# Kernel optimization log

Hardware: AMD Instinct MI355X
Metric: run time of the kernel (lower is better)

## Reference

```python
import jax, jax.numpy as jnp
import numpy as np

B, S, D, H, KH, DH, L, V, MULT = 1, 2048, 2048, 16, 2, 128, 4, 10000, 4
INNER = D * MULT
EPS = 1e-5


def layernorm(x, g, b):
    m = jnp.mean(x, axis=-1, keepdims=True)
    v = jnp.var(x, axis=-1, keepdims=True)
    return (x - m) * jax.lax.rsqrt(v + EPS) * g + b


def setup_inputs() -> dict:
    key = jax.random.key(0)
    ks = jax.random.split(key, 24)
    s = lambda *shape: 0.02
    inp = {
        'text': jax.random.randint(ks[0], (B, S), 0, V),
        'embed_w': jax.random.normal(ks[1], (V, D), jnp.float32) * 0.02,
        # model-level LayerNorm (applied after embed and after every block)
        'model_norm_g': jnp.ones((D,), jnp.float32),
        'model_norm_b': jnp.zeros((D,), jnp.float32),
        # per-block params, stacked on leading L axis
        'blk_norm_g': jnp.ones((L, D), jnp.float32),
        'blk_norm_b': jnp.zeros((L, D), jnp.float32),
        'attn_norm_g': jnp.ones((L, D), jnp.float32),  # RingAttention prenorm
        'attn_norm_b': jnp.zeros((L, D), jnp.float32),
        'wq': jax.random.normal(ks[2], (L, D, H * DH), jnp.float32) * 0.02,
        'wk': jax.random.normal(ks[3], (L, D, KH * DH), jnp.float32) * 0.02,
        'wv': jax.random.normal(ks[4], (L, D, KH * DH), jnp.float32) * 0.02,
        'wo': jax.random.normal(ks[5], (L, H * DH, D), jnp.float32) * 0.02,
        'qn_g': jnp.ones((L, DH), jnp.float32),  # qk_norm LayerNorm scales
        'kn_g': jnp.ones((L, DH), jnp.float32),
        'w1': jax.random.normal(ks[6], (L, D, INNER), jnp.float32) * 0.02,
        'b1': jnp.zeros((L, INNER), jnp.float32),
        'w2': jax.random.normal(ks[7], (L, INNER, D), jnp.float32) * 0.02,
        'b2': jnp.zeros((L, D), jnp.float32),
        # output head: LayerNorm + Linear(D, V)
        'head_norm_g': jnp.ones((D,), jnp.float32),
        'head_norm_b': jnp.zeros((D,), jnp.float32),
        'head_w': jax.random.normal(ks[8], (D, V), jnp.float32) * 0.02,
        'head_b': jnp.zeros((V,), jnp.float32),
    }
    return inp


def _attention(xn, wq, wk, wv, wo, qn_g, kn_g):
    # xn: [B,S,D] (already prenormed)
    q = (xn @ wq).reshape(B, S, H, DH)
    k = (xn @ wk).reshape(B, S, KH, DH)
    v = (xn @ wv).reshape(B, S, KH, DH)
    # qk-norm: LayerNorm over head dim with learnable scale
    q = layernorm(q, qn_g, 0.0)
    k = layernorm(k, kn_g, 0.0)
    # GQA: expand kv heads to query heads
    rep = H // KH
    k = jnp.repeat(k, rep, axis=2)  # [B,S,H,DH]
    v = jnp.repeat(v, rep, axis=2)
    scale = DH ** -0.5
    scores = jnp.einsum('bqhd,bkhd->bhqk', q, k) * scale  # [B,H,S,S]
    causal = jnp.tril(jnp.ones((S, S), bool))
    scores = jnp.where(causal, scores, jnp.finfo(scores.dtype).min)
    p = jax.nn.softmax(scores, axis=-1)
    out = jnp.einsum('bhqk,bkhd->bqhd', p, v).reshape(B, S, H * DH)
    return out @ wo


def reference(text, embed_w, model_norm_g, model_norm_b, blk_norm_g, blk_norm_b,
              attn_norm_g, attn_norm_b, wq, wk, wv, wo, qn_g, kn_g,
              w1, b1, w2, b2, head_norm_g, head_norm_b, head_w, head_b):
    x = embed_w[text]                                # [B,S,D]
    x = layernorm(x, model_norm_g, model_norm_b)
    for i in range(L):
        h = layernorm(x, blk_norm_g[i], blk_norm_b[i])       # block norm
        hn = layernorm(h, attn_norm_g[i], attn_norm_b[i])    # attn prenorm
        h = _attention(hn, wq[i], wk[i], wv[i], wo[i], qn_g[i], kn_g[i]) + h
        ff = jax.nn.gelu(h @ w1[i] + b1[i]) @ w2[i] + b2[i]
        x = ff + h
        x = layernorm(x, model_norm_g, model_norm_b)
    x = layernorm(x, head_norm_g, head_norm_b)
    return x @ head_w + head_b                       # [B,S,V] logits
```

## Files before the change

kernel.cpp:

```cpp
#include <hip/hip_runtime.h>
#include <math.h>

#define S_LEN 2048
#define DMODEL 2048
#define NHEAD 16
#define KVHEAD 2
#define DHEAD 128
#define NLAYER 4
#define VOCAB 10000
#define INNER_DIM 8192
#define LN_EPS 1e-5f
#define VOCAB_PAD 10240
#define QKVN 2560

typedef __attribute__((ext_vector_type(4))) float f32x4;
typedef __attribute__((ext_vector_type(2))) float f32x2;
typedef __attribute__((ext_vector_type(8))) short s16x8;
typedef __attribute__((ext_vector_type(4))) short s16x4;

__device__ __forceinline__ short f2bf(float f) {
  union { float f; unsigned u; } v; v.f = f;
  unsigned r = v.u + 0x7FFFu + ((v.u >> 16) & 1u);
  return (short)(r >> 16);
}
__device__ __forceinline__ float bf2f(short s) {
  union { unsigned u; float f; } v; v.u = ((unsigned)(unsigned short)s) << 16;
  return v.f;
}

__device__ __forceinline__ float gelu_tanh(float x) {
  float z = 0.7978845608028654f * (x + 0.044715f * x * x * x);
  float t = __expf(-2.0f * fabsf(z));
  float th = (1.0f - t) / (1.0f + t);
  th = copysignf(th, z);
  return 0.5f * x * (1.0f + th);
}

__device__ __forceinline__ void glds16(const void* g, void* l) {
  __builtin_amdgcn_global_load_lds(
      (const __attribute__((address_space(1))) unsigned int*)g,
      (__attribute__((address_space(3))) unsigned int*)l, 16, 0, 0);
}

__global__ __launch_bounds__(256)
void wtrans_all(const float* __restrict__ wq, const float* __restrict__ wk,
                const float* __restrict__ wv, const float* __restrict__ wo,
                const float* __restrict__ w1, const float* __restrict__ w2,
                short* __restrict__ wqkvT, short* __restrict__ woT,
                short* __restrict__ w1T, short* __restrict__ w2T) {
  __shared__ float ld[64][65];
  int b = blockIdx.x;
  const float* W; short* WT; int gx, K;
  if (b < 1024)      { W = wq; WT = wqkvT; gx = 32; K = 2048; }
  else if (b < 1152) { b -= 1024; W = wk; WT = wqkvT + (size_t)2048 * 2048; gx = 4; K = 2048; }
  else if (b < 1280) { b -= 1152; W = wv; WT = wqkvT + (size_t)2304 * 2048; gx = 4; K = 2048; }
  else if (b < 2304) { b -= 1280; W = wo; WT = woT; gx = 32; K = 2048; }
  else if (b < 6400) { b -= 2304; W = w1; WT = w1T; gx = 128; K = 2048; }
  else               { b -= 6400; W = w2; WT = w2T; gx = 32; K = 8192; }
  const int N = gx * 64;
  const int n0 = (b % gx) * 64, k0 = (b / gx) * 64;
  const int tid = threadIdx.x;
  const int rbase = tid >> 4;
  const int c4 = (tid & 15) * 4;
#pragma unroll
  for (int q = 0; q < 4; ++q) {
    int kk = rbase + q * 16;
    f32x4 v = *(const f32x4*)(W + (size_t)(k0 + kk) * N + n0 + c4);
    ld[kk][c4 + 0] = v[0]; ld[kk][c4 + 1] = v[1];
    ld[kk][c4 + 2] = v[2]; ld[kk][c4 + 3] = v[3];
  }
  __syncthreads();
#pragma unroll
  for (int s = 0; s < 2; ++s) {
    int lin = tid + s * 256;
    int nn = lin >> 3;
    int ks = lin & 7;
    s16x8 o;
#pragma unroll
    for (int j = 0; j < 8; ++j) o[j] = f2bf(ld[ks * 8 + j][nn]);
    *(s16x8*)&WT[(size_t)(n0 + nn) * K + k0 + ks * 8] = o;
  }
}

__global__ __launch_bounds__(256)
void wtrans64(const float* __restrict__ W, short* __restrict__ WT,
              int K, int N, int NP) {
  __shared__ float ld[64][65];
  const int n0 = blockIdx.x * 64, k0 = blockIdx.y * 64;
  const int tid = threadIdx.x;
  const int rbase = tid >> 4;
  const int c4 = (tid & 15) * 4;
#pragma unroll
  for (int q = 0; q < 4; ++q) {
    int kk = rbase + q * 16;
    const float* wp = W + (size_t)(k0 + kk) * N + n0 + c4;
    float v0, v1, v2, v3;
    if (n0 + c4 + 3 < N) {
      f32x4 v = *(const f32x4*)wp;
      v0 = v[0]; v1 = v[1]; v2 = v[2]; v3 = v[3];
    } else {
      v0 = (n0 + c4 + 0 < N) ? wp[0] : 0.f;
      v1 = (n0 + c4 + 1 < N) ? wp[1] : 0.f;
      v2 = (n0 + c4 + 2 < N) ? wp[2] : 0.f;
      v3 = (n0 + c4 + 3 < N) ? wp[3] : 0.f;
    }
    ld[kk][c4 + 0] = v0; ld[kk][c4 + 1] = v1;
    ld[kk][c4 + 2] = v2; ld[kk][c4 + 3] = v3;
  }
  __syncthreads();
#pragma unroll
  for (int s = 0; s < 2; ++s) {
    int lin = tid + s * 256;
    int nn = lin >> 3;
    int ks = lin & 7;
    int n = n0 + nn;
    if (n < NP) {
      s16x8 o;
#pragma unroll
      for (int j = 0; j < 8; ++j)
        o[j] = (n < N) ? f2bf(ld[ks * 8 + j][nn]) : (short)0;
      *(s16x8*)&WT[(size_t)n * K + k0 + ks * 8] = o;
    }
  }
}

__device__ __forceinline__ void ln3_core(
    float (&v)[8], int tid, int wave,
    const float* __restrict__ mg, const float* __restrict__ mb,
    const float* __restrict__ bg, const float* __restrict__ bb,
    const float* __restrict__ ag, const float* __restrict__ ab,
    short* __restrict__ hbrow, short* __restrict__ hnrow,
    float rs[3][4], float rs2[3][4]) {
#pragma unroll
  for (int rnd = 0; rnd < 3; ++rnd) {
    float s = 0.f, s2 = 0.f;
#pragma unroll
    for (int i = 0; i < 8; ++i) { s += v[i]; s2 += v[i] * v[i]; }
#pragma unroll
    for (int off = 1; off < 64; off <<= 1) {
      s += __shfl_xor(s, off); s2 += __shfl_xor(s2, off);
    }
    if ((tid & 63) == 0) { rs[rnd][wave] = s; rs2[rnd][wave] = s2; }
    __syncthreads();
    s = rs[rnd][0] + rs[rnd][1] + rs[rnd][2] + rs[rnd][3];
    s2 = rs2[rnd][0] + rs2[rnd][1] + rs2[rnd][2] + rs2[rnd][3];
    const float mean = s * (1.f / DMODEL);
    const float var = s2 * (1.f / DMODEL) - mean * mean;
    const float rstd = rsqrtf(var + LN_EPS);
    const float* gg = (rnd == 0) ? mg : (rnd == 1) ? bg : ag;
    const float* bbv = (rnd == 0) ? mb : (rnd == 1) ? bb : ab;
#pragma unroll
    for (int i = 0; i < 8; ++i) {
      int idx = tid + i * 256;
      v[i] = (v[i] - mean) * rstd * gg[idx] + bbv[idx];
    }
    if (rnd == 1) {
#pragma unroll
      for (int i = 0; i < 8; ++i) hbrow[tid + i * 256] = f2bf(v[i]);
    }
  }
#pragma unroll
  for (int i = 0; i < 8; ++i) hnrow[tid + i * 256] = f2bf(v[i]);
}

__global__ __launch_bounds__(256)
void embed_ln3(const int* __restrict__ text, const float* __restrict__ ew,
               const float* __restrict__ mg, const float* __restrict__ mb,
               const float* __restrict__ bg, const float* __restrict__ bb,
               const float* __restrict__ ag, const float* __restrict__ ab,
               short* __restrict__ hb16, short* __restrict__ hn16) {
  const int row = blockIdx.x;
  const int tid = threadIdx.x;
  const int wave = tid >> 6;
  __shared__ float rs[3][4], rs2[3][4];
  float v[8];
  const float* x = ew + (size_t)text[row] * DMODEL;
#pragma unroll
  for (int i = 0; i < 8; ++i) v[i] = x[tid + i * 256];
  ln3_core(v, tid, wave, mg, mb, bg, bb, ag, ab,
           hb16 + (size_t)row * DMODEL, hn16 + (size_t)row * DMODEL, rs, rs2);
}

__global__ __launch_bounds__(256)
void ln_triple_sum(const float* __restrict__ p0, const float* __restrict__ p1,
                   const short* __restrict__ h216, const float* __restrict__ b2,
                   const float* __restrict__ mg, const float* __restrict__ mb,
                   const float* __restrict__ bg, const float* __restrict__ bb,
                   const float* __restrict__ ag, const float* __restrict__ ab,
                   short* __restrict__ hb16, short* __restrict__ hn16) {
  const int row = blockIdx.x;
  const int tid = threadIdx.x;
  const int wave = tid >> 6;
  __shared__ float rs[3][4], rs2[3][4];
  float v[8];
  const size_t base = (size_t)row * DMODEL;
#pragma unroll
  for (int i = 0; i < 8; ++i) {
    int idx = tid + i * 256;
    v[i] = p0[base + idx] + p1[base + idx] + b2[idx] + bf2f(h216[base + idx]);
  }
  ln3_core(v, tid, wave, mg, mb, bg, bb, ag, ab,
           hb16 + base, hn16 + base, rs, rs2);
}

__global__ __launch_bounds__(256)
void ln_dual_sum(const float* __restrict__ p0, const float* __restrict__ p1,
                 const short* __restrict__ h216, const float* __restrict__ b2,
                 const float* __restrict__ mg, const float* __restrict__ mb,
                 const float* __restrict__ hg, const float* __restrict__ hbv,
                 short* __restrict__ out16) {
  const int row = blockIdx.x;
  const int tid = threadIdx.x;
  const int wave = tid >> 6;
  __shared__ float rs[2][4], rs2[2][4];
  float v[8];
  const size_t base = (size_t)row * DMODEL;
#pragma unroll
  for (int i = 0; i < 8; ++i) {
    int idx = tid + i * 256;
    v[i] = p0[base + idx] + p1[base + idx] + b2[idx] + bf2f(h216[base + idx]);
  }
#pragma unroll
  for (int rnd = 0; rnd < 2; ++rnd) {
    float s = 0.f, s2 = 0.f;
#pragma unroll
    for (int i = 0; i < 8; ++i) { s += v[i]; s2 += v[i] * v[i]; }
#pragma unroll
    for (int off = 1; off < 64; off <<= 1) {
      s += __shfl_xor(s, off); s2 += __shfl_xor(s2, off);
    }
    if ((tid & 63) == 0) { rs[rnd][wave] = s; rs2[rnd][wave] = s2; }
    __syncthreads();
    s = rs[rnd][0] + rs[rnd][1] + rs[rnd][2] + rs[rnd][3];
    s2 = rs2[rnd][0] + rs2[rnd][1] + rs2[rnd][2] + rs2[rnd][3];
    const float mean = s * (1.f / DMODEL);
    const float var = s2 * (1.f / DMODEL) - mean * mean;
    const float rstd = rsqrtf(var + LN_EPS);
    const float* gg = (rnd == 0) ? mg : hg;
    const float* bbv = (rnd == 0) ? mb : hbv;
#pragma unroll
    for (int i = 0; i < 8; ++i) {
      int idx = tid + i * 256;
      v[i] = (v[i] - mean) * rstd * gg[idx] + bbv[idx];
    }
  }
  short* o = out16 + base;
#pragma unroll
  for (int i = 0; i < 8; ++i) o[tid + i * 256] = f2bf(v[i]);
}

template<int BM, int BN, int BK, int WM, int WN, int ACT, bool BIAS, bool RESB,
         bool WF, bool WB, bool SPLITK>
__global__ __launch_bounds__(WM * WN * 64)
void gemm_db(const short* __restrict__ A, const short* __restrict__ BT,
             const float* __restrict__ bias, const short* __restrict__ res16,
             float* __restrict__ Cf, short* __restrict__ Cb,
             int M, int N, int K, int LDA, int LDB) {
  constexpr int THREADS = WM * WN * 64;
  constexpr int MR = BM / WM / 16;
  constexpr int NR = BN / WN / 16;
  constexpr int KH = BK / 32;
  constexpr int SLOTS = BK / 8;
  constexpr int SMASK = SLOTS - 1;
  constexpr int RSH = (SLOTS == 8) ? 0 : 1;
  constexpr int CSH = (SLOTS == 8) ? 3 : 2;
  constexpr int NIA = (BM * BK) / (THREADS * 8);
  constexpr int NIB = (BN * BK) / (THREADS * 8);
  __shared__ short As[2][BM * BK];
  __shared__ short Bs[2][BN * BK];
  const int tid = threadIdx.x;
  const int wave = tid >> 6, lane = tid & 63;
  const int g = lane >> 4, r = lane & 15;
  const int wm = wave / WN, wn = wave % WN;
  const int zoff = SPLITK ? blockIdx.z * K : 0;
  if (SPLITK && WF) Cf += (size_t)blockIdx.z * M * N;

  const int GY = gridDim.y;
  int lin = blockIdx.x + blockIdx.y * gridDim.x;
  int nwg = gridDim.x * GY;
  int sw = ((nwg & 7) == 0) ? ((lin & 7) * (nwg >> 3) + (lin >> 3)) : lin;
  const int bm = (sw % GY) * BM;
  const int bn = (sw / GY) * BN;

  const short* gsrc[NIA + NIB];
  short* ldst[2][NIA + NIB];
#pragma unroll
  for (int i = 0; i < NIA; ++i) {
    int c = i * THREADS + tid;
    int row = c >> CSH;
    int slot = c & SMASK;
    int col = ((slot ^ ((row >> RSH) & SMASK)) << 3);
    gsrc[i] = A + (size_t)(bm + row) * LDA + zoff + col;
    int base = (i * THREADS + (wave << 6)) << 3;
    ldst[0][i] = &As[0][base];
    ldst[1][i] = &As[1][base];
  }
#pragma unroll
  for (int i = 0; i < NIB; ++i) {
    int c = i * THREADS + tid;
    int row = c >> CSH;
    int slot = c & SMASK;
    int col = ((slot ^ ((row >> RSH) & SMASK)) << 3);
    gsrc[NIA + i] = BT + (size_t)(bn + row) * LDB + zoff + col;
    int base = (i * THREADS + (wave << 6)) << 3;
    ldst[0][NIA + i] = &Bs[0][base];
    ldst[1][NIA + i] = &Bs[1][base];
  }

  f32x4 acc[MR][NR] = {};
  const int NT = K / BK;

#pragma unroll
  for (int i = 0; i < NIA + NIB; ++i) glds16(gsrc[i], ldst[0][i]);
  asm volatile("s_waitcnt vmcnt(0)" ::: "memory");
  __syncthreads();

  for (int t = 0; t < NT; ++t) {
    const int cur = t & 1;
    const short* as = As[cur];
    const short* bs = Bs[cur];
    s16x8 bfr[NR][KH], af[(MR > 1) ? MR / 2 : 1][KH];
#pragma unroll
    for (int n = 0; n < NR; ++n) {
      int rr = wn * (NR * 16) + n * 16 + r;
#pragma unroll
      for (int kk = 0; kk < KH; ++kk) {
        int lg = kk * 4 + g;
        bfr[n][kk] = *(const s16x8*)&bs[rr * BK + ((lg ^ ((rr >> RSH) & SMASK)) << 3)];
      }
    }
#pragma unroll
    for (int mm = 0; mm < MR / 2; ++mm) {
      int rr = wm * (MR * 16) + mm * 16 + r;
#pragma unroll
      for (int kk = 0; kk < KH; ++kk) {
        int lg = kk * 4 + g;
        af[mm][kk] = *(const s16x8*)&as[rr * BK + ((lg ^ ((rr >> RSH) & SMASK)) << 3)];
      }
    }
    if (t + 1 < NT) {
#pragma unroll
      for (int i = 0; i < NIA + NIB; ++i) glds16(gsrc[i] + (t + 1) * BK, ldst[cur ^ 1][i]);
    }
    asm volatile("s_waitcnt lgkmcnt(0)" ::: "memory");
    __builtin_amdgcn_sched_barrier(0);
    __builtin_amdgcn_s_setprio(1);
#pragma unroll
    for (int mm = 0; mm < MR / 2; ++mm)
#pragma unroll
      for (int n = 0; n < NR; ++n)
#pragma unroll
        for (int kk = 0; kk < KH; ++kk)
          acc[mm][n] = __builtin_amdgcn_mfma_f32_16x16x32_bf16(af[mm][kk], bfr[n][kk], acc[mm][n], 0, 0, 0);
    __builtin_amdgcn_s_setprio(0);
    __builtin_amdgcn_s_barrier();
#pragma unroll
    for (int mm = 0; mm < MR / 2; ++mm) {
      int rr = wm * (MR * 16) + (MR / 2 + mm) * 16 + r;
#pragma unroll
      for (int kk = 0; kk < KH; ++kk) {
        int lg = kk * 4 + g;
        af[mm][kk] = *(const s16x8*)&as[rr * BK + ((lg ^ ((rr >> RSH) & SMASK)) << 3)];
      }
    }
    asm volatile("s_waitcnt lgkmcnt(0)" ::: "memory");
    __builtin_amdgcn_sched_barrier(0);
    __builtin_amdgcn_s_setprio(1);
#pragma unroll
    for (int mm = 0; mm < MR / 2; ++mm)
#pragma unroll
      for (int n = 0; n < NR; ++n)
#pragma unroll
        for (int kk = 0; kk < KH; ++kk)
          acc[MR / 2 + mm][n] = __builtin_amdgcn_mfma_f32_16x16x32_bf16(af[mm][kk], bfr[n][kk], acc[MR / 2 + mm][n], 0, 0, 0);
    __builtin_amdgcn_s_setprio(0);
    __syncthreads();
  }

#pragma unroll
  for (int m = 0; m < MR; ++m) {
    int row = bm + wm * (MR * 16) + m * 16 + g * 4;
#pragma unroll
    for (int n = 0; n < NR; ++n) {
      int col = bn + wn * (NR * 16) + n * 16 + r;
      if (col < N) {
#pragma unroll
        for (int j = 0; j < 4; ++j) {
          float v = acc[m][n][j];
          if (BIAS) v += bias[col];
          if (ACT) v = gelu_tanh(v);
          if (RESB) v += bf2f(res16[(size_t)(row + j) * N + col]);
          if (WF) Cf[(size_t)(row + j) * N + col] = v;
          if (WB) Cb[(size_t)(row + j) * N + col] = f2bf(v);
        }
      }
    }
  }
}

__global__ __launch_bounds__(256)
void gemm_qkv(const short* __restrict__ A, const short* __restrict__ BT,
              const float* __restrict__ qg, const float* __restrict__ kg,
              short* __restrict__ qb, short* __restrict__ kb,
              short* __restrict__ vt, int M, int K) {
  __shared__ short As[2][64 * 64];
  __shared__ short Bs[2][128 * 64];
  __shared__ float rsm[2][64], rs2m[2][64];
  const int tid = threadIdx.x;
  const int wave = tid >> 6, lane = tid & 63;
  const int g = lane >> 4, r = lane & 15;
  const int wm = wave >> 1, wn = wave & 1;

  const int GY = gridDim.y;
  int lin = blockIdx.x + blockIdx.y * gridDim.x;
  int nwg = gridDim.x * GY;
  int sw = (lin & 7) * (nwg >> 3) + (lin >> 3);
  const int bm = (sw % GY) * 64;
  const int bn = (sw / GY) * 128;

  const short* gsrc[6];
  short* ldst[2][6];
#pragma unroll
  for (int i = 0; i < 2; ++i) {
    int c = i * 256 + tid;
    int row = c >> 3, slot = c & 7;
    int col = ((slot ^ (row & 7)) << 3);
    gsrc[i] = A + (size_t)(bm + row) * K + col;
    int base = (i * 256 + (wave << 6)) << 3;
    ldst[0][i] = &As[0][base];
    ldst[1][i] = &As[1][base];
  }
#pragma unroll
  for (int i = 0; i < 4; ++i) {
    int c = i * 256 + tid;
    int row = c >> 3, slot = c & 7;
    int col = ((slot ^ (row & 7)) << 3);
    gsrc[2 + i] = BT + (size_t)(bn + row) * K + col;
    int base = (i * 256 + (wave << 6)) << 3;
    ldst[0][2 + i] = &Bs[0][base];
    ldst[1][2 + i] = &Bs[1][base];
  }

  f32x4 acc[2][4] = {};
  const int NT = K >> 6;

#pragma unroll
  for (int i = 0; i < 6; ++i) glds16(gsrc[i], ldst[0][i]);
  asm volatile("s_waitcnt vmcnt(0)" ::: "memory");
  __syncthreads();

  for (int t = 0; t < NT; ++t) {
    const int cur = t & 1;
    const short* as = As[cur];
    const short* bs = Bs[cur];
    s16x8 bfr[4][2], af[1][2];
#pragma unroll
    for (int n = 0; n < 4; ++n) {
      int rr = wn * 64 + n * 16 + r;
#pragma unroll
      for (int kk = 0; kk < 2; ++kk) {
        int lg = kk * 4 + g;
        bfr[n][kk] = *(const s16x8*)&bs[rr * 64 + ((lg ^ (rr & 7)) << 3)];
      }
    }
    {
      int rr = wm * 32 + r;
#pragma unroll
      for (int kk = 0; kk < 2; ++kk) {
        int lg = kk * 4 + g;
        af[0][kk] = *(const s16x8*)&as[rr * 64 + ((lg ^ (rr & 7)) << 3)];
      }
    }
    if (t + 1 < NT) {
#pragma unroll
      for (int i = 0; i < 6; ++i) glds16(gsrc[i] + (t + 1) * 64, ldst[cur ^ 1][i]);
    }
    asm volatile("s_waitcnt lgkmcnt(0)" ::: "memory");
    __builtin_amdgcn_sched_barrier(0);
    __builtin_amdgcn_s_setprio(1);
#pragma unroll
    for (int n = 0; n < 4; ++n)
#pragma unroll
      for (int kk = 0; kk < 2; ++kk)
        acc[0][n] = __builtin_amdgcn_mfma_f32_16x16x32_bf16(af[0][kk], bfr[n][kk], acc[0][n], 0, 0, 0);
    __builtin_amdgcn_s_setprio(0);
    __builtin_amdgcn_s_barrier();
    {
      int rr = wm * 32 + 16 + r;
#pragma unroll
      for (int kk = 0; kk < 2; ++kk) {
        int lg = kk * 4 + g;
        af[0][kk] = *(const s16x8*)&as[rr * 64 + ((lg ^ (rr & 7)) << 3)];
      }
    }
    asm volatile("s_waitcnt lgkmcnt(0)" ::: "memory");
    __builtin_amdgcn_sched_barrier(0);
    __builtin_amdgcn_s_setprio(1);
#pragma unroll
    for (int n = 0; n < 4; ++n)
#pragma unroll
      for (int kk = 0; kk < 2; ++kk)
        acc[1][n] = __builtin_amdgcn_mfma_f32_16x16x32_bf16(af[0][kk], bfr[n][kk], acc[1][n], 0, 0, 0);
    __builtin_amdgcn_s_setprio(0);
    __syncthreads();
  }

  if (bn >= 2304) {
    short* ld = &As[0][0];
#pragma unroll
    for (int m = 0; m < 2; ++m) {
      int sl = wm * 32 + m * 16 + g * 4;
#pragma unroll
      for (int n = 0; n < 4; ++n) {
        int dl = wn * 64 + n * 16 + r;
#pragma unroll
        for (int j = 0; j < 4; ++j)
          ld[(sl + j) * 128 + dl] = f2bf(acc[m][n][j]);
      }
    }
    __syncthreads();
    const int dl = tid & 127;
    const int sh = (tid >> 7) * 32;
    short* dst = vt + (size_t)(bn - 2304 + dl) * S_LEN + bm + sh;
#pragma unroll
    for (int v = 0; v < 4; ++v) {
      s16x8 o;
#pragma unroll
      for (int i = 0; i < 8; ++i) o[i] = ld[(sh + v * 8 + i) * 128 + dl];
      *(s16x8*)(dst + v * 8) = o;
    }
  } else {
    float ms[2][4], m2[2][4];
#pragma unroll
    for (int m = 0; m < 2; ++m)
#pragma unroll
      for (int j = 0; j < 4; ++j) {
        float s = 0.f, s2 = 0.f;
#pragma unroll
        for (int n = 0; n < 4; ++n) { float v = acc[m][n][j]; s += v; s2 += v * v; }
#pragma unroll
        for (int off = 1; off < 16; off <<= 1) {
          s += __shfl_xor(s, off); s2 += __shfl_xor(s2, off);
        }
        ms[m][j] = s; m2[m][j] = s2;
      }
    if (r == 0) {
#pragma unroll
      for (int m = 0; m < 2; ++m)
#pragma unroll
        for (int j = 0; j < 4; ++j) {
          int rl = wm * 32 + m * 16 + g * 4 + j;
          rsm[wn][rl] = ms[m][j]; rs2m[wn][rl] = m2[m][j];
        }
    }
    __syncthreads();
    const float* gv = (bn < 2048) ? qg : kg;
#pragma unroll
    for (int m = 0; m < 2; ++m)
#pragma unroll
      for (int j = 0; j < 4; ++j) {
        int rl = wm * 32 + m * 16 + g * 4 + j;
        float s = rsm[0][rl] + rsm[1][rl];
        float s2 = rs2m[0][rl] + rs2m[1][rl];
        float mean = s * (1.f / 128.f);
        float var = s2 * (1.f / 128.f) - mean * mean;
        float rstd = rsqrtf(var + LN_EPS);
        int srow = bm + rl;
#pragma unroll
        for (int n = 0; n < 4; ++n) {
          int cl = wn * 64 + n * 16 + r;
          float v = (acc[m][n][j] - mean) * rstd * gv[cl];
          if (bn < 2048) qb[(size_t)srow * 2048 + bn + cl] = f2bf(v);
          else kb[(size_t)srow * 256 + (bn - 2048) + cl] = f2bf(v);
        }
      }
  }
}

__global__ __launch_bounds__(256)
void attn_fwd3(const short* __restrict__ qbuf, const short* __restrict__ kbuf,
               const short* __restrict__ vtb, short* __restrict__ obuf) {
  __shared__ short Qs[64 * 128];
  __shared__ short Ks[64 * 128];
  __shared__ short Vt[128 * 64];
  __shared__ short Ps[4][16][88];
  const int tid = threadIdx.x;
  int lin = blockIdx.x + blockIdx.y * gridDim.x;
  int sw = (lin & 7) * 32 + (lin >> 3);
  const int pair = sw & 15;
  const int h = sw >> 4;
  const int kh = h >> 3;
  const int wave = tid >> 6, lane = tid & 63;
  const int g = lane >> 4, r = lane & 15;
  const float scale = 0.08838834764831845f;

#pragma unroll
  for (int half = 0; half < 2; ++half) {
    const int qt = half ? (31 - pair) : pair;
    const int qbase = qt * 64;
    __builtin_amdgcn_s_barrier();
#pragma unroll
    for (int i = 0; i < 4; ++i) {
      int c = i * 256 + tid;
      int row = c >> 4;
      int scol = (((c & 15) ^ (row & 7)) << 3);
      glds16(qbuf + (size_t)(qbase + row) * DMODEL + h * DHEAD + scol,
             &Qs[(i * 256 + (wave << 6)) << 3]);
    }
    f32x4 O[8] = {};
    float mst[4], lst[4];
#pragma unroll
    for (int j = 0; j < 4; ++j) { mst[j] = -1e30f; lst[j] = 0.f; }
    s16x8 aq[4];

    for (int jt = 0; jt <= qt; ++jt) {
      const int jb = jt * 64;
      if (jt) __builtin_amdgcn_s_barrier();
#pragma unroll
      for (int i = 0; i < 4; ++i) {
        int c = i * 256 + tid;
        int row = c >> 4;
        int scol = (((c & 15) ^ (row & 7)) << 3);
        glds16(kbuf + (size_t)(jb + row) * 256 + kh * DHEAD + scol,
               &Ks[(i * 256 + (wave << 6)) << 3]);
      }
#pragma unroll
      for (int i = 0; i < 4; ++i) {
        int c = i * 256 + tid;
        int row = c >> 3;
        int scol = (((c & 7) ^ (row & 7)) << 3);
        glds16(vtb + (size_t)(kh * 128 + row) * S_LEN + jb + scol,
               &Vt[(i * 256 + (wave << 6)) << 3]);
      }
      asm volatile("s_waitcnt vmcnt(4)" ::: "memory");
      __builtin_amdgcn_s_barrier();
      if (jt == 0) {
#pragma unroll
        for (int kc = 0; kc < 4; ++kc) {
          int rr = wave * 16 + r;
          aq[kc] = *(const s16x8*)&Qs[rr * 128 + ((((kc << 2) | g) ^ (rr & 7)) << 3)];
        }
      }
      f32x4 sc[4] = {};
      __builtin_amdgcn_s_setprio(1);
#pragma unroll
      for (int n = 0; n < 4; ++n) {
        int rr = n * 16 + r;
#pragma unroll
        for (int kc = 0; kc < 4; ++kc) {
          s16x8 bk = *(const s16x8*)&Ks[rr * 128 + ((((kc << 2) | g) ^ (rr & 7)) << 3)];
          sc[n] = __builtin_amdgcn_mfma_f32_16x16x32_bf16(aq[kc], bk, sc[n], 0, 0, 0);
        }
      }
      __builtin_amdgcn_s_setprio(0);
      if (jt == qt) {
#pragma unroll
        for (int j = 0; j < 4; ++j) {
          int irow = qbase + wave * 16 + g * 4 + j;
#pragma unroll
          for (int n = 0; n < 4; ++n) {
            int jcol = jb + n * 16 + r;
            sc[n][j] = (jcol <= irow) ? sc[n][j] * scale : -1e30f;
          }
        }
      } else {
#pragma unroll
        for (int j = 0; j < 4; ++j)
#pragma unroll
          for (int n = 0; n < 4; ++n) sc[n][j] *= scale;
      }
      float pmax[4], alpha[4], rsum[4];
#pragma unroll
      for (int j = 0; j < 4; ++j)
        pmax[j] = fmaxf(fmaxf(sc[0][j], sc[1][j]), fmaxf(sc[2][j], sc[3][j]));
#pragma unroll
      for (int off = 1; off < 16; off <<= 1)
#pragma unroll
        for (int j = 0; j < 4; ++j) pmax[j] = fmaxf(pmax[j], __shfl_xor(pmax[j], off));
#pragma unroll
      for (int j = 0; j < 4; ++j) {
        float mnew = fmaxf(mst[j], pmax[j]);
        alpha[j] = __expf(mst[j] - mnew);
        mst[j] = mnew;
#pragma unroll
        for (int n = 0; n < 4; ++n) sc[n][j] = __expf(sc[n][j] - mnew);
        rsum[j] = (sc[0][j] + sc[1][j]) + (sc[2][j] + sc[3][j]);
      }
#pragma unroll
      for (int off = 1; off < 16; off <<= 1)
#pragma unroll
        for (int j = 0; j < 4; ++j) rsum[j] += __shfl_xor(rsum[j], off);
#pragma unroll
      for (int j = 0; j < 4; ++j) lst[j] = lst[j] * alpha[j] + rsum[j];
#pragma unroll
      for (int d = 0; d < 8; ++d)
#pragma unroll
        for (int j = 0; j < 4; ++j) O[d][j] *= alpha[j];
      asm volatile("s_waitcnt vmcnt(0)" ::: "memory");
      __builtin_amdgcn_s_barrier();
#pragma unroll
      for (int j = 0; j < 4; ++j)
#pragma unroll
        for (int n = 0; n < 4; ++n)
          Ps[wave][g * 4 + j][n * 16 + r] = f2bf(sc[n][j]);
      s16x8 pa0 = *(const s16x8*)&Ps[wave][r][g * 8];
      s16x8 pa1 = *(const s16x8*)&Ps[wave][r][32 + g * 8];
      __builtin_amdgcn_s_setprio(1);
#pragma unroll
      for (int d = 0; d < 8; ++d) {
        int dd = d * 16 + r;
        s16x8 b0 = *(const s16x8*)&Vt[dd * 64 + ((g ^ (dd & 7)) << 3)];
        s16x8 b1 = *(const s16x8*)&Vt[dd * 64 + (((4 + g) ^ (dd & 7)) << 3)];
        O[d] = __builtin_amdgcn_mfma_f32_16x16x32_bf16(pa0, b0, O[d], 0, 0, 0);
        O[d] = __builtin_amdgcn_mfma_f32_16x16x32_bf16(pa1, b1, O[d], 0, 0, 0);
      }
      __builtin_amdgcn_s_setprio(0);
    }
    float linv[4];
#pragma unroll
    for (int j = 0; j < 4; ++j) linv[j] = 1.f / lst[j];
#pragma unroll
    for (int d = 0; d < 8; ++d)
#pragma unroll
      for (int j = 0; j < 4; ++j)
        obuf[(size_t)(qbase + wave * 16 + g * 4 + j) * DMODEL + h * DHEAD + d * 16 + r] =
            f2bf(O[d][j] * linv[j]);
  }
}

extern "C" void kernel_launch(void* const* d_in, const int* in_sizes, int n_in,
                              void* d_out, int out_size, void* d_ws, size_t ws_size,
                              hipStream_t stream) {
  const int* text = (const int*)d_in[0];
  const float* embed_w = (const float*)d_in[1];
  const float* model_g = (const float*)d_in[2];
  const float* model_b = (const float*)d_in[3];
  const float* blk_g = (const float*)d_in[4];
  const float* blk_b = (const float*)d_in[5];
  const float* attn_g = (const float*)d_in[6];
  const float* attn_b = (const float*)d_in[7];
  const float* wq = (const float*)d_in[8];
  const float* wk = (const float*)d_in[9];
  const float* wv = (const float*)d_in[10];
  const float* wo = (const float*)d_in[11];
  const float* qn_g = (const float*)d_in[12];
  const float* kn_g = (const float*)d_in[13];
  const float* w1 = (const float*)d_in[14];
  const float* b1 = (const float*)d_in[15];
  const float* w2 = (const float*)d_in[16];
  const float* b2 = (const float*)d_in[17];
  const float* head_g = (const float*)d_in[18];
  const float* head_b = (const float*)d_in[19];
  const float* head_w = (const float*)d_in[20];
  const float* head_bias = (const float*)d_in[21];
  float* out = (float*)d_out;

  const size_t SD = (size_t)S_LEN * DMODEL;
  const size_t SKV = (size_t)S_LEN * KVHEAD * DHEAD;
  const size_t SI = (size_t)S_LEN * INNER_DIM;
  const size_t WD = (size_t)DMODEL * DMODEL;
  const size_t WKV = (size_t)DMODEL * KVHEAD * DHEAD;
  const size_t WI = (size_t)DMODEL * INNER_DIM;

  char* p = (char*)d_ws;
  float* wpart = (float*)p; p += SD * 4 * 2;
  short* hb16  = (short*)p; p += SD * 2;
  short* hn16  = (short*)p; p += SD * 2;
  short* h216  = (short*)p; p += SD * 2;
  short* ao16  = (short*)p; p += SD * 2;
  short* ffi16 = (short*)p; p += SI * 2;
  short* qb16  = (short*)p; p += SD * 2;
  short* kb16  = (short*)p; p += SKV * 2;
  short* vt16  = (short*)p; p += SKV * 2;
  short* wqkvT = (short*)p; p += (size_t)QKVN * DMODEL * 2;
  short* woT   = (short*)p; p += WD * 2;
  short* w1T   = (short*)p; p += WI * 2;
  short* w2T   = (short*)p; p += WI * 2;
  short* headT = w1T;

  dim3 blk(256);
  embed_ln3<<<S_LEN, blk, 0, stream>>>(text, embed_w, model_g, model_b,
                                       blk_g, blk_b, attn_g, attn_b, hb16, hn16);

  for (int i = 0; i < NLAYER; ++i) {
    wtrans_all<<<10496, blk, 0, stream>>>(
        wq + (size_t)i * WD, wk + (size_t)i * WKV, wv + (size_t)i * WKV,
        wo + (size_t)i * WD, w1 + (size_t)i * WI, w2 + (size_t)i * WI,
        wqkvT, woT, w1T, w2T);

    gemm_qkv<<<dim3(QKVN / 128, S_LEN / 64), blk, 0, stream>>>(
        hn16, wqkvT, qn_g + i * DHEAD, kn_g + i * DHEAD,
        qb16, kb16, vt16, S_LEN, DMODEL);

    attn_fwd3<<<dim3(16, 16), blk, 0, stream>>>(qb16, kb16, vt16, ao16);

    gemm_db<64, 128, 64, 2, 2, 0, false, true, false, true, false>
        <<<dim3(DMODEL / 128, S_LEN / 64), blk, 0, stream>>>(
        ao16, woT, nullptr, hb16, nullptr, h216,
        S_LEN, DMODEL, DMODEL, DMODEL, DMODEL);
    gemm_db<128, 128, 64, 2, 2, 1, true, false, false, true, false>
        <<<dim3(INNER_DIM / 128, S_LEN / 128), blk, 0, stream>>>(
        h216, w1T, b1 + (size_t)i * INNER_DIM, nullptr, nullptr, ffi16,
        S_LEN, INNER_DIM, DMODEL, DMODEL, DMODEL);
    gemm_db<128, 128, 64, 2, 2, 0, false, false, true, false, true>
        <<<dim3(DMODEL / 128, S_LEN / 128, 2), blk, 0, stream>>>(
        ffi16, w2T, nullptr, nullptr, wpart, nullptr,
        S_LEN, DMODEL, INNER_DIM / 2, INNER_DIM, INNER_DIM);

    if (i + 1 < NLAYER) {
      ln_triple_sum<<<S_LEN, blk, 0, stream>>>(
          wpart, wpart + SD, h216, b2 + (size_t)i * DMODEL,
          model_g, model_b,
          blk_g + (i + 1) * DMODEL, blk_b + (i + 1) * DMODEL,
          attn_g + (i + 1) * DMODEL, attn_b + (i + 1) * DMODEL, hb16, hn16);
    } else {
      ln_dual_sum<<<S_LEN, blk, 0, stream>>>(
          wpart, wpart + SD, h216, b2 + (size_t)i * DMODEL,
          model_g, model_b, head_g, head_b, hn16);
    }
  }

  wtrans64<<<dim3(VOCAB_PAD / 64, 32), blk, 0, stream>>>(head_w, headT, DMODEL, VOCAB, VOCAB_PAD);
  gemm_db<128, 128, 64, 2, 2, 0, true, false, true, false, false>
      <<<dim3(VOCAB_PAD / 128, S_LEN / 128), blk, 0, stream>>>(
      hn16, headT, head_bias, nullptr, out, nullptr,
      S_LEN, VOCAB, DMODEL, DMODEL, DMODEL);
}
```

Measured before the change: 1.476 ms.

## Replace double-buffered GEMM LDS pipeline with single-buffer synchronous loads

Converts the GEMM kernels (generic and QKV) from double-buffered shared memory with prefetch of the next K tile overlapped with MFMA into a single buffer that loads, waits, syncs, then computes. It also drops the split A-fragment scheduling, setprio hints and sched barriers. The change halves LDS use, which could allow more resident workgroups per CU, but it removes overlap of global loads with compute and adds an extra barrier per iteration.

```diff
diff --git a/kernel.cpp b/kernel.cpp
--- a/kernel.cpp
+++ b/kernel.cpp
@@ -252,7 +252,7 @@
 template<int BM, int BN, int BK, int WM, int WN, int ACT, bool BIAS, bool RESB,
          bool WF, bool WB, bool SPLITK>
 __global__ __launch_bounds__(WM * WN * 64)
-void gemm_db(const short* __restrict__ A, const short* __restrict__ BT,
+void gemm_sb(const short* __restrict__ A, const short* __restrict__ BT,
              const float* __restrict__ bias, const short* __restrict__ res16,
              float* __restrict__ Cf, short* __restrict__ Cb,
              int M, int N, int K, int LDA, int LDB) {
@@ -266,8 +266,8 @@
   constexpr int CSH = (SLOTS == 8) ? 3 : 2;
   constexpr int NIA = (BM * BK) / (THREADS * 8);
   constexpr int NIB = (BN * BK) / (THREADS * 8);
-  __shared__ short As[2][BM * BK];
-  __shared__ short Bs[2][BN * BK];
+  __shared__ short As[BM * BK];
+  __shared__ short Bs[BN * BK];
   const int tid = threadIdx.x;
   const int wave = tid >> 6, lane = tid & 63;
   const int g = lane >> 4, r = lane & 15;
@@ -283,7 +283,7 @@
   const int bn = (sw / GY) * BN;
 
   const short* gsrc[NIA + NIB];
-  short* ldst[2][NIA + NIB];
+  short* ldst[NIA + NIB];
 #pragma unroll
   for (int i = 0; i < NIA; ++i) {
     int c = i * THREADS + tid;
@@ -291,9 +291,7 @@
     int slot = c & SMASK;
     int col = ((slot ^ ((row >> RSH) & SMASK)) << 3);
     gsrc[i] = A + (size_t)(bm + row) * LDA + zoff + col;
-    int base = (i * THREADS + (wave << 6)) << 3;
-    ldst[0][i] = &As[0][base];
-    ldst[1][i] = &As[1][base];
+    ldst[i] = &As[(i * THREADS + (wave << 6)) << 3];
   }
 #pragma unroll
   for (int i = 0; i < NIB; ++i) {
@@ -302,79 +300,44 @@
     int slot = c & SMASK;
     int col = ((slot ^ ((row >> RSH) & SMASK)) << 3);
     gsrc[NIA + i] = BT + (size_t)(bn + row) * LDB + zoff + col;
-    int base = (i * THREADS + (wave << 6)) << 3;
-    ldst[0][NIA + i] = &Bs[0][base];
-    ldst[1][NIA + i] = &Bs[1][base];
+    ldst[NIA + i] = &Bs[(i * THREADS + (wave << 6)) << 3];
   }
 
   f32x4 acc[MR][NR] = {};
   const int NT = K / BK;
 
-#pragma unroll
-  for (int i = 0; i < NIA + NIB; ++i) glds16(gsrc[i], ldst[0][i]);
-  asm volatile("s_waitcnt vmcnt(0)" ::: "memory");
-  __syncthreads();
-
   for (int t = 0; t < NT; ++t) {
-    const int cur = t & 1;
-    const short* as = As[cur];
-    const short* bs = Bs[cur];
-    s16x8 bfr[NR][KH], af[(MR > 1) ? MR / 2 : 1][KH];
+    if (t) __syncthreads();
+#pragma unroll
+    for (int i = 0; i < NIA + NIB; ++i) glds16(gsrc[i] + t * BK, ldst[i]);
+    asm volatile("s_waitcnt vmcnt(0)" ::: "memory");
+    __syncthreads();
+    s16x8 af[MR][KH], bf[NR][KH];
+#pragma unroll
+    for (int m = 0; m < MR; ++m) {
+      int rr = wm * (MR * 16) + m * 16 + r;
+#pragma unroll
+      for (int kk = 0; kk < KH; ++kk) {
+        int lg = kk * 4 + g;
+        af[m][kk] = *(const s16x8*)&As[rr * BK + ((lg ^ ((rr >> RSH) & SMASK)) << 3)];
+      }
+    }
 #pragma unroll
     for (int n = 0; n < NR; ++n) {
       int rr = wn * (NR * 16) + n * 16 + r;
 #pragma unroll
       for (int kk = 0; kk < KH; ++kk) {
         int lg = kk * 4 + g;
-        bfr[n][kk] = *(const s16x8*)&bs[rr * BK + ((lg ^ ((rr >> RSH) & SMASK)) << 3)];
-      }
-    }
-#pragma unroll
-    for (int mm = 0; mm < MR / 2; ++mm) {
-      int rr = wm * (MR * 16) + mm * 16 + r;
-#pragma unroll
-      for (int kk = 0; kk < KH; ++kk) {
-        int lg = kk * 4 + g;
-        af[mm][kk] = *(const s16x8*)&as[rr * BK + ((lg ^ ((rr >> RSH) & SMASK)) << 3)];
-      }
-    }
-    if (t + 1 < NT) {
-#pragma unroll
-      for (int i = 0; i < NIA + NIB; ++i) glds16(gsrc[i] + (t + 1) * BK, ldst[cur ^ 1][i]);
-    }
-    asm volatile("s_waitcnt lgkmcnt(0)" ::: "memory");
-    __builtin_amdgcn_sched_barrier(0);
-    __builtin_amdgcn_s_setprio(1);
-#pragma unroll
-    for (int mm = 0; mm < MR / 2; ++mm)
+        bf[n][kk] = *(const s16x8*)&Bs[rr * BK + ((lg ^ ((rr >> RSH) & SMASK)) << 3)];
+      }
+    }
+#pragma unroll
+    for (int m = 0; m < MR; ++m)
 #pragma unroll
       for (int n = 0; n < NR; ++n)
 #pragma unroll
         for (int kk = 0; kk < KH; ++kk)
-          acc[mm][n] = __builtin_amdgcn_mfma_f32_16x16x32_bf16(af[mm][kk], bfr[n][kk], acc[mm][n], 0, 0, 0);
-    __builtin_amdgcn_s_setprio(0);
-    __builtin_amdgcn_s_barrier();
-#pragma unroll
-    for (int mm = 0; mm < MR / 2; ++mm) {
-      int rr = wm * (MR * 16) + (MR / 2 + mm) * 16 + r;
-#pragma unroll
-      for (int kk = 0; kk < KH; ++kk) {
-        int lg = kk * 4 + g;
-        af[mm][kk] = *(const s16x8*)&as[rr * BK + ((lg ^ ((rr >> RSH) & SMASK)) << 3)];
-      }
-    }
-    asm volatile("s_waitcnt lgkmcnt(0)" ::: "memory");
-    __builtin_amdgcn_sched_barrier(0);
-    __builtin_amdgcn_s_setprio(1);
-#pragma unroll
-    for (int mm = 0; mm < MR / 2; ++mm)
-#pragma unroll
-      for (int n = 0; n < NR; ++n)
-#pragma unroll
-        for (int kk = 0; kk < KH; ++kk)
-          acc[MR / 2 + mm][n] = __builtin_amdgcn_mfma_f32_16x16x32_bf16(af[mm][kk], bfr[n][kk], acc[MR / 2 + mm][n], 0, 0, 0);
-    __builtin_amdgcn_s_setprio(0);
-    __syncthreads();
+          acc[m][n] = __builtin_amdgcn_mfma_f32_16x16x32_bf16(af[m][kk], bf[n][kk], acc[m][n], 0, 0, 0);
   }
 
 #pragma unroll
@@ -403,8 +366,8 @@
               const float* __restrict__ qg, const float* __restrict__ kg,
               short* __restrict__ qb, short* __restrict__ kb,
               short* __restrict__ vt, int M, int K) {
-  __shared__ short As[2][64 * 64];
-  __shared__ short Bs[2][128 * 64];
+  __shared__ short As[64 * 64];
+  __shared__ short Bs[128 * 64];
   __shared__ float rsm[2][64], rs2m[2][64];
   const int tid = threadIdx.x;
   const int wave = tid >> 6, lane = tid & 63;
@@ -419,16 +382,14 @@
   const int bn = (sw / GY) * 128;
 
   const short* gsrc[6];
-  short* ldst[2][6];
+  short* ldst[6];
 #pragma unroll
   for (int i = 0; i < 2; ++i) {
     int c = i * 256 + tid;
     int row = c >> 3, slot = c & 7;
     int col = ((slot ^ (row & 7)) << 3);
     gsrc[i] = A + (size_t)(bm + row) * K + col;
-    int base = (i * 256 + (wave << 6)) << 3;
-    ldst[0][i] = &As[0][base];
-    ldst[1][i] = &As[1][base];
+    ldst[i] = &As[(i * 256 + (wave << 6)) << 3];
   }
 #pragma unroll
   for (int i = 0; i < 4; ++i) {
@@ -436,77 +397,49 @@
     int row = c >> 3, slot = c & 7;
     int col = ((slot ^ (row & 7)) << 3);
     gsrc[2 + i] = BT + (size_t)(bn + row) * K + col;
-    int base = (i * 256 + (wave << 6)) << 3;
-    ldst[0][2 + i] = &Bs[0][base];
-    ldst[1][2 + i] = &Bs[1][base];
+    ldst[2 + i] = &Bs[(i * 256 + (wave << 6)) << 3];
   }
 
   f32x4 acc[2][4] = {};
   const int NT = K >> 6;
 
-#pragma unroll
-  for (int i = 0; i < 6; ++i) glds16(gsrc[i], ldst[0][i]);
-  asm volatile("s_waitcnt vmcnt(0)" ::: "memory");
-  __syncthreads();
-
   for (int t = 0; t < NT; ++t) {
-    const int cur = t & 1;
-    const short* as = As[cur];
-    const short* bs = Bs[cur];
-    s16x8 bfr[4][2], af[1][2];
+    if (t) __syncthreads();
+#pragma unroll
+    for (int i = 0; i < 6; ++i) glds16(gsrc[i] + t * 64, ldst[i]);
+    asm volatile("s_waitcnt vmcnt(0)" ::: "memory");
+    __syncthreads();
+    s16x8 af[2][2], bf[4][2];
+#pragma unroll
+    for (int m = 0; m < 2; ++m) {
+      int rr = wm * 32 + m * 16 + r;
+#pragma unroll
+      for (int kk = 0; kk < 2; ++kk) {
+        int lg = kk * 4 + g;
+        af[m][kk] = *(const s16x8*)&As[rr * 64 + ((lg ^ (rr & 7)) << 3)];
+      }
+    }
 #pragma unroll
     for (int n = 0; n < 4; ++n) {
       int rr = wn * 64 + n * 16 + r;
 #pragma unroll
       for (int kk = 0; kk < 2; ++kk) {
         int lg = kk * 4 + g;
-        bfr[n][kk] = *(const s16x8*)&bs[rr * 64 + ((lg ^ (rr & 7)) << 3)];
-      }
-    }
-    {
-      int rr = wm * 32 + r;
-#pragma unroll
-      for (int kk = 0; kk < 2; ++kk) {
-        int lg = kk * 4 + g;
-        af[0][kk] = *(const s16x8*)&as[rr * 64 + ((lg ^ (rr & 7)) << 3)];
-      }
-    }
-    if (t + 1 < NT) {
-#pragma unroll
-      for (int i = 0; i < 6; ++i) glds16(gsrc[i] + (t + 1) * 64, ldst[cur ^ 1][i]);
-    }
-    asm volatile("s_waitcnt lgkmcnt(0)" ::: "memory");
-    __builtin_amdgcn_sched_barrier(0);
-    __builtin_amdgcn_s_setprio(1);
-#pragma unroll
-    for (int n = 0; n < 4; ++n)
-#pragma unroll
-      for (int kk = 0; kk < 2; ++kk)
-        acc[0][n] = __builtin_amdgcn_mfma_f32_16x16x32_bf16(af[0][kk], bfr[n][kk], acc[0][n], 0, 0, 0);
-    __builtin_amdgcn_s_setprio(0);
-    __builtin_amdgcn_s_barrier();
-    {
-      int rr = wm * 32 + 16 + r;
-#pragma unroll
-      for (int kk = 0; kk < 2; ++kk) {
-        int lg = kk * 4 + g;
-        af[0][kk] = *(const s16x8*)&as[rr * 64 + ((lg ^ (rr & 7)) << 3)];
-      }
-    }
-    asm volatile("s_waitcnt lgkmcnt(0)" ::: "memory");
-    __builtin_amdgcn_sched_barrier(0);
-    __builtin_amdgcn_s_setprio(1);
-#pragma unroll
-    for (int n = 0; n < 4; ++n)
-#pragma unroll
-      for (int kk = 0; kk < 2; ++kk)
-        acc[1][n] = __builtin_amdgcn_mfma_f32_16x16x32_bf16(af[0][kk], bfr[n][kk], acc[1][n], 0, 0, 0);
-    __builtin_amdgcn_s_setprio(0);
+        bf[n][kk] = *(const s16x8*)&Bs[rr * 64 + ((lg ^ (rr & 7)) << 3)];
+      }
+    }
+#pragma unroll
+    for (int m = 0; m < 2; ++m)
+#pragma unroll
+      for (int n = 0; n < 4; ++n)
+#pragma unroll
+        for (int kk = 0; kk < 2; ++kk)
+          acc[m][n] = __builtin_amdgcn_mfma_f32_16x16x32_bf16(af[m][kk], bf[n][kk], acc[m][n], 0, 0, 0);
+  }
+
+  if (bn >= 2304) {
     __syncthreads();
-  }
-
-  if (bn >= 2304) {
-    short* ld = &As[0][0];
+    short* ld = &Bs[0];
 #pragma unroll
     for (int m = 0; m < 2; ++m) {
       int sl = wm * 32 + m * 16 + g * 4;
@@ -794,15 +727,15 @@
 
     attn_fwd3<<<dim3(16, 16), blk, 0, stream>>>(qb16, kb16, vt16, ao16);
 
-    gemm_db<64, 128, 64, 2, 2, 0, false, true, false, true, false>
+    gemm_sb<64, 128, 64, 2, 2, 0, false, true, false, true, false>
         <<<dim3(DMODEL / 128, S_LEN / 64), blk, 0, stream>>>(
         ao16, woT, nullptr, hb16, nullptr, h216,
         S_LEN, DMODEL, DMODEL, DMODEL, DMODEL);
-    gemm_db<128, 128, 64, 2, 2, 1, true, false, false, true, false>
+    gemm_sb<128, 128, 64, 2, 2, 1, true, false, false, true, false>
         <<<dim3(INNER_DIM / 128, S_LEN / 128), blk, 0, stream>>>(
         h216, w1T, b1 + (size_t)i * INNER_DIM, nullptr, nullptr, ffi16,
         S_LEN, INNER_DIM, DMODEL, DMODEL, DMODEL);
-    gemm_db<128, 128, 64, 2, 2, 0, false, false, true, false, true>
+    gemm_sb<128, 128, 64, 2, 2, 0, false, false, true, false, true>
         <<<dim3(DMODEL / 128, S_LEN / 128, 2), blk, 0, stream>>>(
         ffi16, w2T, nullptr, nullptr, wpart, nullptr,
         S_LEN, DMODEL, INNER_DIM / 2, INNER_DIM, INNER_DIM);
@@ -821,7 +754,7 @@
   }
 
   wtrans64<<<dim3(VOCAB_PAD / 64, 32), blk, 0, stream>>>(head_w, headT, DMODEL, VOCAB, VOCAB_PAD);
-  gemm_db<128, 128, 64, 2, 2, 0, true, false, true, false, false>
+  gemm_sb<128, 128, 64, 2, 2, 0, true, false, true, false, false>
       <<<dim3(VOCAB_PAD / 128, S_LEN / 128), blk, 0, stream>>>(
       hn16, headT, head_bias, nullptr, out, nullptr,
       S_LEN, VOCAB, DMODEL, DMODEL, DMODEL);
```

New measurement: 1.523 ms. 3.2% more time.
